# Performance work log

Measured on AMD Instinct MI355X. Metric: run time of the kernel, lower is better.

## Reference

```python
import jax, jax.numpy as jnp
import numpy as np

G = 512          # graphs in batch
NPG = 128        # nodes per graph (equal-sized so decoder batches)
TEMP = 0.1       # SimilarityDecoder temperature


def setup_inputs() -> dict:
    key = jax.random.key(0)
    ks = jax.random.split(key, 10)
    N, D, K, H, T = G * NPG, 512, 1024, 128, 10
    return {
        "x": jax.random.normal(ks[0], (N, D), jnp.float32),
        "batch": jnp.repeat(jnp.arange(G, dtype=jnp.int64), NPG),
        "codebook_input": jax.random.normal(ks[1], (K, D), jnp.float32),
        "fc1_w": jax.random.normal(ks[2], (H, D), jnp.float32) * (1.0 / np.sqrt(D)),
        "fc1_b": jax.random.normal(ks[3], (H,), jnp.float32) * 0.01,
        "fc2_w": jax.random.normal(ks[4], (D, H), jnp.float32) * (1.0 / np.sqrt(H)),
        "fc2_b": jax.random.normal(ks[5], (D,), jnp.float32) * 0.01,
        "causal": jax.random.normal(ks[6], (K, K), jnp.float32),
        "cls_w": jax.random.normal(ks[7], (T, D), jnp.float32) * (1.0 / np.sqrt(D)),
        "cls_b": jax.random.normal(ks[8], (T,), jnp.float32) * 0.01,
    }


def _segment_mean(v, batch, num_segments):
    s = jax.ops.segment_sum(v, batch, num_segments=num_segments)
    cnt = jax.ops.segment_sum(jnp.ones((v.shape[0], 1), v.dtype), batch, num_segments=num_segments)
    return s / jnp.maximum(cnt, 1.0)


def _batched_adj(z):
    # SimilarityDecoder: per-graph sigmoid(norm_z @ norm_z.T / temp); graphs equal-sized -> [G, n, n]
    zg = z.reshape(G, NPG, -1)
    zn = zg / jnp.maximum(jnp.linalg.norm(zg, axis=-1, keepdims=True), 1e-12)
    return jax.nn.sigmoid(jnp.einsum("gnd,gmd->gnm", zn, zn) / TEMP)


def reference(x, batch, codebook_input, fc1_w, fc1_b, fc2_w, fc2_b, causal, cls_w, cls_b):
    K = causal.shape[0]
    I = jnp.eye(K, dtype=x.dtype)

    # ---- VectorQuantizer ----
    h = jax.nn.sigmoid(codebook_input @ fc1_w.T + fc1_b)
    codebook_transformed = h @ fc2_w.T + fc2_b                 # [K, D]
    causal_effect = causal * (1.0 - I) + I                     # off-diag causal + identity
    cs = jax.nn.sigmoid(codebook_transformed)
    causal_diag = causal * I
    causal_cb = causal_effect @ (causal_diag @ cs)             # [K, D]
    counter_matrix = causal * (1.0 - I)                        # DegreeLayer assumed: off-diagonal mask
    counter_cb = causal_effect @ (counter_matrix @ cs)         # [K, D]

    # ---- ClassLayer ----
    pooled_x = _segment_mean(x, batch, G)                      # [G, D]
    # squared euclidean distances x vs causal_cb -> argmin codebook index
    d2 = (jnp.sum(x * x, 1, keepdims=True)
          - 2.0 * (x @ causal_cb.T)
          + jnp.sum(causal_cb * causal_cb, 1))                 # [N, K]
    idx = jnp.argmin(d2, axis=1)                               # [N]
    causal_nodes = x + causal_cb[idx]
    counter_nodes = counter_cb[idx]
    z_nodes = codebook_transformed[idx]                        # [N, D]
    pooled_causal = _segment_mean(causal_nodes, batch, G)
    pooled_counter = _segment_mean(counter_nodes, batch, G)
    causal_pre = pooled_causal @ cls_w.T + cls_b
    counter_pre = pooled_counter @ cls_w.T + cls_b
    y_pre = pooled_x @ jax.lax.stop_gradient(cls_w).T + jax.lax.stop_gradient(cls_b)

    # ---- SimilarityDecoder ----
    A_ori = _batched_adj(x)                                    # [G, n, n]
    A_rec = _batched_adj(z_nodes)

    return (causal_pre, counter_pre, y_pre, A_ori, A_rec,
            z_nodes, x, causal_diag, counter_matrix, pooled_causal, pooled_x)
```

## Files before the change

### kernel.cpp

```cpp
#include <hip/hip_runtime.h>
#include <math.h>

#define NG   512
#define NPG  128
#define NN   65536
#define DD   512
#define KK   1024
#define HH   128
#define TT   10

#define RES_TAU 1.0f
#define RES_CAP 65536

typedef __attribute__((ext_vector_type(8))) short short8;
typedef __attribute__((ext_vector_type(4))) float float4v;

static const long OFF_CPRE = 0;
static const long OFF_KPRE = 5120;
static const long OFF_YPRE = 10240;
static const long OFF_AORI = 15360;
static const long OFF_AREC = OFF_AORI + 8388608L;
static const long OFF_Z    = OFF_AREC + 8388608L;
static const long OFF_X    = OFF_Z + 33554432L;
static const long OFF_CD   = OFF_X + 33554432L;
static const long OFF_CM   = OFF_CD + 1048576L;
static const long OFF_PC   = OFF_CM + 1048576L;
static const long OFF_PX   = OFF_PC + 262144L;

__device__ __forceinline__ float sigm_fast(float v) { return 1.0f / (1.0f + __expf(-v)); }
__device__ __forceinline__ float sigm_acc (float v) { return 1.0f / (1.0f + expf(-v)); }

__global__ void k_diagmask(const float* __restrict__ causal,
                           float* __restrict__ cd, float* __restrict__ cm,
                           float* __restrict__ dv) {
  int i = blockIdx.x * 256 + threadIdx.x;
  int r = i >> 10, c = i & 1023;
  float v = causal[i];
  bool diag = (r == c);
  cd[i] = diag ? v : 0.0f;
  cm[i] = diag ? 0.0f : v;
  if (diag) dv[r] = v;
}

__global__ void k_fc1(const float* __restrict__ cbi, const float* __restrict__ w,
                      const float* __restrict__ b, float* __restrict__ h) {
  int i = blockIdx.x * 256 + threadIdx.x;
  int k = i >> 7, j = i & 127;
  const float4* xr = (const float4*)(cbi + (long)k * DD);
  const float4* wr = (const float4*)(w + (long)j * DD);
  float s = b[j];
  for (int d = 0; d < DD / 4; d++) {
    float4 a = xr[d], bb = wr[d];
    s += a.x * bb.x + a.y * bb.y + a.z * bb.z + a.w * bb.w;
  }
  h[i] = sigm_acc(s);
}

__global__ void k_fc2(const float* __restrict__ h, const float* __restrict__ w,
                      const float* __restrict__ b, float* __restrict__ ct,
                      float* __restrict__ cs) {
  int i = blockIdx.x * 256 + threadIdx.x;
  int k = i >> 9, d = i & 511;
  const float4* hr = (const float4*)(h + (long)k * HH);
  const float4* wr = (const float4*)(w + (long)d * HH);
  float s = b[d];
  for (int j = 0; j < HH / 4; j++) {
    float4 a = hr[j], bb = wr[j];
    s += a.x * bb.x + a.y * bb.y + a.z * bb.z + a.w * bb.w;
  }
  ct[i] = s;
  cs[i] = sigm_acc(s);
}

template <int AM, int BM>
__launch_bounds__(256)
__global__ void gemm64(const float* __restrict__ A, const float* __restrict__ B,
                       const float* __restrict__ dscale, float* __restrict__ C,
                       int M, int Nc, int Kr) {
  __shared__ __align__(16) float as[32][68];
  __shared__ __align__(16) float bs[32][68];
  int tid = threadIdx.x;
  int tx = tid & 15, ty = tid >> 4;
  int m0 = blockIdx.y * 64, n0 = blockIdx.x * 64;
  float acc[4][4] = {};
  for (int kt = 0; kt < Kr; kt += 32) {
    for (int s = tid; s < 512; s += 256) {
      int m = s >> 3, c4 = (s & 7) << 2;
      int gr = m0 + m, gc = kt + c4;
      float4 v = *(const float4*)&A[(long)gr * Kr + gc];
      float vv[4] = {v.x, v.y, v.z, v.w};
      if (AM == 1) {
#pragma unroll
        for (int q = 0; q < 4; q++) if (gc + q == gr) vv[q] = 1.0f;
      } else if (AM == 2) {
#pragma unroll
        for (int q = 0; q < 4; q++) if (gc + q == gr) vv[q] = 0.0f;
      }
      as[c4 + 0][m] = vv[0]; as[c4 + 1][m] = vv[1];
      as[c4 + 2][m] = vv[2]; as[c4 + 3][m] = vv[3];
    }
    for (int s = tid; s < 512; s += 256) {
      int r = s >> 4, c4 = (s & 15) << 2;
      float4 v = *(const float4*)&B[(long)(kt + r) * Nc + n0 + c4];
      if (BM == 1) {
        float sc = dscale[kt + r];
        v.x *= sc; v.y *= sc; v.z *= sc; v.w *= sc;
      }
      *(float4*)&bs[r][c4] = v;
    }
    __syncthreads();
#pragma unroll
    for (int r = 0; r < 32; r++) {
      float4 a4 = *(const float4*)&as[r][ty * 4];
      float4 b4 = *(const float4*)&bs[r][tx * 4];
      float av[4] = {a4.x, a4.y, a4.z, a4.w};
      float bv[4] = {b4.x, b4.y, b4.z, b4.w};
#pragma unroll
      for (int i = 0; i < 4; i++)
#pragma unroll
        for (int j = 0; j < 4; j++) acc[i][j] += av[i] * bv[j];
    }
    __syncthreads();
  }
#pragma unroll
  for (int i = 0; i < 4; i++) {
    float4 v = make_float4(acc[i][0], acc[i][1], acc[i][2], acc[i][3]);
    *(float4*)&C[(long)(m0 + ty * 4 + i) * Nc + n0 + tx * 4] = v;
  }
}

__global__ void k_cnorm(const float* __restrict__ ccb, float* __restrict__ cn2,
                        int* __restrict__ rc) {
  if (blockIdx.x == 0 && threadIdx.x == 0) *rc = 0;
  int row = blockIdx.x * 4 + (threadIdx.x >> 6);
  int lane = threadIdx.x & 63;
  const float* r = ccb + (long)row * DD;
  float s = 0.0f;
  for (int q = 0; q < DD; q += 64) { float v = r[lane + q]; s += v * v; }
  for (int off = 32; off > 0; off >>= 1) s += __shfl_down(s, off);
  if (lane == 0) cn2[row] = s;
}

__device__ __forceinline__ ushort bf16_rne(float f, float* back) {
  unsigned int b = __float_as_uint(f);
  unsigned int r = b + 0x7fffu + ((b >> 16) & 1u);
  ushort h = (ushort)(r >> 16);
  *back = __uint_as_float(((unsigned int)h) << 16);
  return h;
}

__global__ void k_split(const float4* __restrict__ src, ushort* __restrict__ hi,
                        ushort* __restrict__ lo, long n4) {
  long i = (long)blockIdx.x * 256 + threadIdx.x;
  if (i >= n4) return;
  float4 v = src[i];
  float vv[4] = {v.x, v.y, v.z, v.w};
  ushort h[4], l[4];
#pragma unroll
  for (int q = 0; q < 4; q++) {
    float back;
    h[q] = bf16_rne(vv[q], &back);
    float rem = vv[q] - back;
    float dummy;
    l[q] = bf16_rne(rem, &dummy);
  }
  ((ushort4*)hi)[i] = make_ushort4(h[0], h[1], h[2], h[3]);
  ((ushort4*)lo)[i] = make_ushort4(l[0], l[1], l[2], l[3]);
}

__launch_bounds__(512, 2)
__global__ void k_argmin_mfma(const ushort* __restrict__ xh, const ushort* __restrict__ xl,
                              const ushort* __restrict__ ch, const ushort* __restrict__ cl,
                              const float* __restrict__ cn2, int* __restrict__ idxg,
                              int* __restrict__ rc, int* __restrict__ rlist) {
  __shared__ __align__(16) ushort xsh[64 * 512];
  __shared__ __align__(16) ushort xsl[64 * 512];
  __shared__ float cn2s[KK];
  __shared__ float mm1[8][64], mm2[8][64];
  __shared__ int   mid[8][64];

  int tid = threadIdx.x;
  long n0 = (long)blockIdx.x * 64;

  uint4 tmp[16];
#pragma unroll
  for (int r = 0; r < 16; r++) {
    int g = tid + r * 512;
    int rid = g >> 6;
    int node = rid & 63;
    int gb = (g & 63) << 4;
    const ushort* src = ((rid < 64) ? xh : xl) + (n0 + node) * (long)DD;
    tmp[r] = *(const uint4*)((const char*)src + gb);
  }
  for (int s = tid; s < KK; s += 512) cn2s[s] = cn2[s];
#pragma unroll
  for (int r = 0; r < 16; r++) {
    int g = tid + r * 512;
    int rid = g >> 6;
    int node = rid & 63;
    int gb = (g & 63) << 4;
    int db = gb ^ ((node & 7) << 4);
    ushort* dst = (rid < 64) ? xsh : xsl;
    *(uint4*)((char*)dst + node * 1024 + db) = tmp[r];
  }
  __syncthreads();

  int lane = tid & 63, wave = tid >> 6;
  int col = lane & 15, quad = lane >> 4;

  int abase[4];
#pragma unroll
  for (int i = 0; i < 4; i++) {
    int node = i * 16 + col;
    abase[i] = node * 1024 + ((quad ^ (node & 3)) << 4) + (((node >> 2) & 1) << 6);
  }

  const ushort* pBh[4];
  const ushort* pBl[4];
#pragma unroll
  for (int j = 0; j < 4; j++) {
    long row = (long)(wave * 64 + j * 16 + col);
    pBh[j] = ch + row * DD + quad * 8;
    pBl[j] = cl + row * DD + quad * 8;
  }

  float m1[16], m2[16]; int id1[16];
#pragma unroll
  for (int s = 0; s < 16; s++) { m1[s] = 3.4e38f; m2[s] = 3.4e38f; id1[s] = 0; }

  const float4v vzero = {0.0f, 0.0f, 0.0f, 0.0f};
  float4v acc[4][4];
  short8 ahA[4], alA[4], bhA[4], blA[4];
  short8 ahB[4], alB[4], bhB[4], blB[4];

#define PREF(K, AH, AL, BH, BL)                                                  \
  do {                                                                           \
    int k_ = (K);                                                                \
    _Pragma("unroll") for (int j = 0; j < 4; j++) {                              \
      BH[j] = *(const short8*)(pBh[j] + k_ * 32);                                \
      BL[j] = *(const short8*)(pBl[j] + k_ * 32);                                \
    }                                                                            \
    _Pragma("unroll") for (int i = 0; i < 4; i++) {                              \
      int ao_ = abase[i] ^ (k_ << 6);                                            \
      AH[i] = *(const short8*)((const char*)xsh + ao_);                          \
      AL[i] = *(const short8*)((const char*)xsl + ao_);                          \
    }                                                                            \
  } while (0)

#define COMP(AH, AL, BH, BL)                                                     \
  do {                                                                           \
    __builtin_amdgcn_s_setprio(1);                                               \
    _Pragma("unroll") for (int j = 0; j < 4; j++)                                \
      _Pragma("unroll") for (int i = 0; i < 4; i++) {                            \
        acc[i][j] = __builtin_amdgcn_mfma_f32_16x16x32_bf16(AH[i], BH[j], acc[i][j], 0, 0, 0); \
        acc[i][j] = __builtin_amdgcn_mfma_f32_16x16x32_bf16(AH[i], BL[j], acc[i][j], 0, 0, 0); \
        acc[i][j] = __builtin_amdgcn_mfma_f32_16x16x32_bf16(AL[i], BH[j], acc[i][j], 0, 0, 0); \
      }                                                                          \
    __builtin_amdgcn_s_setprio(0);                                               \
  } while (0)

  for (int cc = 0; cc < 2; cc++) {
#pragma unroll
    for (int i = 0; i < 4; i++)
#pragma unroll
      for (int j = 0; j < 4; j++) acc[i][j] = vzero;

    PREF(0, ahA, alA, bhA, blA);
#pragma unroll 1
    for (int k = 0; k < 16; k += 2) {
      PREF(k + 1, ahB, alB, bhB, blB);
      COMP(ahA, alA, bhA, blA);
      PREF((k + 2) & 15, ahA, alA, bhA, blA);
      COMP(ahB, alB, bhB, blB);
    }

    int cb0 = cc * 512 + wave * 64;
#pragma unroll
    for (int j = 0; j < 4; j++) {
      int code = cb0 + j * 16 + col;
      float c2 = cn2s[code];
#pragma unroll
      for (int i = 0; i < 4; i++) {
#pragma unroll
        for (int r = 0; r < 4; r++) {
          float v = fmaf(-2.0f, acc[i][j][r], c2);
          int s = i * 4 + r;
          if (v < m1[s] || (v == m1[s] && code < id1[s])) {
            m2[s] = m1[s]; m1[s] = v; id1[s] = code;
          } else if (v < m2[s]) {
            m2[s] = v;
          }
        }
      }
    }
#pragma unroll
    for (int j = 0; j < 4; j++) { pBh[j] += 512 * DD; pBl[j] += 512 * DD; }
  }
#undef PREF
#undef COMP

#pragma unroll
  for (int s = 0; s < 16; s++) {
#pragma unroll
    for (int mask = 1; mask <= 8; mask <<= 1) {
      float om1 = __shfl_xor(m1[s], mask);
      float om2 = __shfl_xor(m2[s], mask);
      int   oid = __shfl_xor(id1[s], mask);
      if (om1 < m1[s] || (om1 == m1[s] && oid < id1[s])) {
        m2[s] = fminf(m1[s], om2); m1[s] = om1; id1[s] = oid;
      } else {
        m2[s] = fminf(m2[s], om1);
      }
    }
  }
  if (col == 0) {
#pragma unroll
    for (int s = 0; s < 16; s++) {
      int i = s >> 2, r = s & 3;
      int nl = i * 16 + quad * 4 + r;
      mm1[wave][nl] = m1[s]; mm2[wave][nl] = m2[s]; mid[wave][nl] = id1[s];
    }
  }
  __syncthreads();
  if (tid < 64) {
    float f1 = mm1[0][tid], f2 = mm2[0][tid]; int fi = mid[0][tid];
#pragma unroll
    for (int w = 1; w < 8; w++) {
      float b1 = mm1[w][tid], b2 = mm2[w][tid]; int bi = mid[w][tid];
      if (b1 < f1 || (b1 == f1 && bi < fi)) {
        f2 = fminf(f1, b2); f1 = b1; fi = bi;
      } else {
        f2 = fminf(f2, b1);
      }
    }
    idxg[n0 + tid] = fi;
    if (f2 - f1 < RES_TAU) {
      int p = atomicAdd(rc, 1);
      if (p < RES_CAP) rlist[p] = (int)(n0 + tid);
    }
  }
}

__global__ void k_rescue(const float* __restrict__ x, const float* __restrict__ ccb,
                         const float* __restrict__ cn2, const int* __restrict__ rc,
                         const int* __restrict__ rlist, int* __restrict__ idxg) {
  __shared__ float xs[DD];
  __shared__ float bv[256]; __shared__ int bi[256];
  int count = *rc; if (count > RES_CAP) count = RES_CAP;
  int tid = threadIdx.x;
  for (int f = blockIdx.x; f < count; f += gridDim.x) {
    int n = rlist[f];
    for (int s = tid; s < DD; s += 256) xs[s] = x[(long)n * DD + s];
    __syncthreads();
    float best = 3.4e38f; int besti = 0;
    for (int c = tid; c < KK; c += 256) {
      const float4* cr = (const float4*)(ccb + (long)c * DD);
      const float4* xr = (const float4*)xs;
      float dot = 0.0f;
      for (int d = 0; d < DD / 4; d++) {
        float4 a = xr[d], b = cr[d];
        dot += a.x * b.x + a.y * b.y + a.z * b.z + a.w * b.w;
      }
      float v = cn2[c] - 2.0f * dot;
      if (v < best || (v == best && c < besti)) { best = v; besti = c; }
    }
    bv[tid] = best; bi[tid] = besti;
    __syncthreads();
    for (int off = 128; off > 0; off >>= 1) {
      if (tid < off) {
        float ov = bv[tid + off]; int oi = bi[tid + off];
        if (ov < bv[tid] || (ov == bv[tid] && oi < bi[tid])) { bv[tid] = ov; bi[tid] = oi; }
      }
      __syncthreads();
    }
    if (tid == 0) idxg[n] = bi[0];
    __syncthreads();
  }
}

__global__ void k_gather(const float4* __restrict__ ct4, const int* __restrict__ idxg,
                         float4* __restrict__ z4) {
  long i = (long)blockIdx.x * 256 + threadIdx.x;
  int n = (int)(i >> 7), c = (int)(i & 127);
  z4[i] = ct4[(long)idxg[n] * 128 + c];
}

__global__ void k_pool(const float* __restrict__ x, const float* __restrict__ ccb,
                       const float* __restrict__ kcb, const int* __restrict__ idxg,
                       float* __restrict__ px, float* __restrict__ pc,
                       float* __restrict__ pk) {
  __shared__ int sidx[NPG];
  int g = blockIdx.x, tid = threadIdx.x;
  if (tid < NPG) sidx[tid] = idxg[g * NPG + tid];
  __syncthreads();
  int d = tid;
  float sx = 0.0f, sc = 0.0f, sk = 0.0f;
  for (int n = 0; n < NPG; n++) {
    sx += x[((long)g * NPG + n) * DD + d];
    long r = (long)sidx[n] * DD + d;
    sc += ccb[r]; sk += kcb[r];
  }
  px[(long)g * DD + d] = sx / 128.0f;
  pc[(long)g * DD + d] = (sx + sc) / 128.0f;
  pk[(long)g * DD + d] = sk / 128.0f;
}

__global__ void k_heads(const float* __restrict__ pc, const float* __restrict__ pk,
                        const float* __restrict__ px, const float* __restrict__ w,
                        const float* __restrict__ b, float* __restrict__ cpre,
                        float* __restrict__ kpre, float* __restrict__ ypre) {
  int g = blockIdx.x, t = threadIdx.x;
  if (t >= 30) return;
  int which = t / 10, tt = t % 10;
  const float* src = (which == 0) ? pc : ((which == 1) ? pk : px);
  const float* sr = src + (long)g * DD;
  const float* wr = w + (long)tt * DD;
  float s = 0.0f;
  for (int d = 0; d < DD; d++) s += sr[d] * wr[d];
  s += b[tt];
  float* dst = (which == 0) ? cpre : ((which == 1) ? kpre : ypre);
  dst[g * TT + tt] = s;
}

__global__ void k_copy(const float4* __restrict__ src, float4* __restrict__ dst) {
  long i = (long)blockIdx.x * 256 + threadIdx.x;
  dst[i] = src[i];
}

__launch_bounds__(256)
__global__ void k_adj(const float* __restrict__ Z, float* __restrict__ Aout) {
  __shared__ float nrm[NPG];
  __shared__ float inv[NPG];
  __shared__ __align__(16) float zs[32][132];
  int tid = threadIdx.x;
  int g = blockIdx.x;
  const float* base = Z + (long)g * NPG * DD;
  if (tid < NPG) nrm[tid] = 0.0f;
  __syncthreads();
  for (int k = 0; k < 64; k++) {
    long i = (long)k * 256 + tid;
    int n = (int)(i >> 7);
    float4 v = ((const float4*)base)[i];
    float s = v.x * v.x + v.y * v.y + v.z * v.z + v.w * v.w;
    for (int off = 32; off > 0; off >>= 1) s += __shfl_down(s, off);
    if ((tid & 63) == 0) atomicAdd(&nrm[n], s);
  }
  __syncthreads();
  if (tid < NPG) inv[tid] = 1.0f / fmaxf(sqrtf(nrm[tid]), 1e-12f);
  __syncthreads();
  float acc[8][8] = {};
  int tx = tid & 15, ty = tid >> 4;
  for (int dt = 0; dt < DD; dt += 32) {
    for (int s = tid; s < 1024; s += 256) {
      int n = s >> 3, c4 = (s & 7) << 2;
      float4 v = *(const float4*)&base[(long)n * DD + dt + c4];
      float iv = inv[n];
      zs[c4 + 0][n] = v.x * iv; zs[c4 + 1][n] = v.y * iv;
      zs[c4 + 2][n] = v.z * iv; zs[c4 + 3][n] = v.w * iv;
    }
    __syncthreads();
#pragma unroll 8
    for (int r = 0; r < 32; r++) {
      float rv[8], cv[8];
      *(float4*)&rv[0] = *(const float4*)&zs[r][ty * 8];
      *(float4*)&rv[4] = *(const float4*)&zs[r][ty * 8 + 4];
      *(float4*)&cv[0] = *(const float4*)&zs[r][tx * 8];
      *(float4*)&cv[4] = *(const float4*)&zs[r][tx * 8 + 4];
#pragma unroll
      for (int i = 0; i < 8; i++)
#pragma unroll
        for (int j = 0; j < 8; j++) acc[i][j] += rv[i] * cv[j];
    }
    __syncthreads();
  }
  float* aout = Aout + (long)g * NPG * NPG;
#pragma unroll
  for (int i = 0; i < 8; i++) {
    int rr = ty * 8 + i;
    float o[8];
#pragma unroll
    for (int j = 0; j < 8; j++) o[j] = sigm_fast(acc[i][j] * 10.0f);
    *(float4*)&aout[(long)rr * NPG + tx * 8]     = make_float4(o[0], o[1], o[2], o[3]);
    *(float4*)&aout[(long)rr * NPG + tx * 8 + 4] = make_float4(o[4], o[5], o[6], o[7]);
  }
}

extern "C" void kernel_launch(void* const* d_in, const int* in_sizes, int n_in,
                              void* d_out, int out_size, void* d_ws, size_t ws_size,
                              hipStream_t stream) {
  const float* x      = (const float*)d_in[0];
  const float* cbi    = (const float*)d_in[2];
  const float* fc1w   = (const float*)d_in[3];
  const float* fc1b   = (const float*)d_in[4];
  const float* fc2w   = (const float*)d_in[5];
  const float* fc2b   = (const float*)d_in[6];
  const float* causal = (const float*)d_in[7];
  const float* clsw   = (const float*)d_in[8];
  const float* clsb   = (const float*)d_in[9];
  float* out = (float*)d_out;

  float* cpre = out + OFF_CPRE;
  float* kpre = out + OFF_KPRE;
  float* ypre = out + OFF_YPRE;

  float* scr  = out + OFF_AORI;
  float* h    = scr;
  float* cs   = scr + 131072L;
  float* tmp2 = scr + 655360L;
  float* ccb  = scr + 1179648L;
  float* kcb  = scr + 1703936L;
  float* cn2  = scr + 2228224L;
  int*   idxg = (int*)(scr + 2229248L);
  float* pk   = scr + 2294784L;
  float* dv   = scr + 2556928L;
  ushort* ch  = (ushort*)(scr + 2557952L);
  ushort* cl  = (ushort*)(scr + 2820096L);
  int*   rc   = (int*)(scr + 3082240L);
  int*   rlist= (int*)(scr + 3082496L);
  float* ct   = out + OFF_AREC;
  ushort* xh  = (ushort*)(out + OFF_X);
  ushort* xl  = (ushort*)(out + OFF_X + 16777216L);

  k_diagmask<<<4096, 256, 0, stream>>>(causal, out + OFF_CD, out + OFF_CM, dv);
  k_fc1<<<512, 256, 0, stream>>>(cbi, fc1w, fc1b, h);
  k_fc2<<<2048, 256, 0, stream>>>(h, fc2w, fc2b, ct, cs);
  gemm64<2, 0><<<dim3(8, 16), 256, 0, stream>>>(causal, cs,   nullptr, tmp2, KK, DD, KK);
  gemm64<1, 1><<<dim3(8, 16), 256, 0, stream>>>(causal, cs,   dv,      ccb,  KK, DD, KK);
  gemm64<1, 0><<<dim3(8, 16), 256, 0, stream>>>(causal, tmp2, nullptr, kcb,  KK, DD, KK);
  k_cnorm<<<256, 256, 0, stream>>>(ccb, cn2, rc);
  k_split<<<32768, 256, 0, stream>>>((const float4*)x, xh, xl, 8388608L);
  k_split<<<512, 256, 0, stream>>>((const float4*)ccb, ch, cl, 131072L);
  k_argmin_mfma<<<1024, 512, 0, stream>>>(xh, xl, ch, cl, cn2, idxg, rc, rlist);
  k_rescue<<<128, 256, 0, stream>>>(x, ccb, cn2, rc, rlist, idxg);
  k_gather<<<32768, 256, 0, stream>>>((const float4*)ct, idxg, (float4*)(out + OFF_Z));
  k_pool<<<512, 512, 0, stream>>>(x, ccb, kcb, idxg, out + OFF_PX, out + OFF_PC, pk);
  k_heads<<<512, 64, 0, stream>>>(out + OFF_PC, pk, out + OFF_PX, clsw, clsb, cpre, kpre, ypre);
  k_copy<<<32768, 256, 0, stream>>>((const float4*)x, (float4*)(out + OFF_X));
  k_adj<<<512, 256, 0, stream>>>(out + OFF_Z, out + OFF_AREC);
  k_adj<<<512, 256, 0, stream>>>(x, out + OFF_AORI);
}
```

Baseline: 1.745 ms.

## Fuse two causal GEMMs, add nontemporal copies, restructure argmin MFMA pipeline

Two GEMMs that share the same causal matrix and cs operand are merged into one dual-accumulator kernel. Inside it, the A tile is masked once for the off-diagonal product and once for the identity diagonal, with a per-k scale applied to B. The x split and copy kernels and the argmin x loads now use nontemporal loads and stores to reduce cache pollution. The argmin inner loop is reorganised to load the A fragments from LDS just before use and to double-buffer only the B fragments, with sched_barriers fixing the order of loads and MFMAs. This lowers register pressure but gives the scheduler less freedom to interleave work.

```diff
diff --git a/kernel.cpp b/kernel.cpp
--- a/kernel.cpp
+++ b/kernel.cpp
@@ -14,6 +14,9 @@
 
 typedef __attribute__((ext_vector_type(8))) short short8;
 typedef __attribute__((ext_vector_type(4))) float float4v;
+typedef __attribute__((ext_vector_type(4))) float        f32x4;
+typedef __attribute__((ext_vector_type(4))) unsigned int u32x4;
+typedef __attribute__((ext_vector_type(4))) unsigned short u16x4;
 
 static const long OFF_CPRE = 0;
 static const long OFF_KPRE = 5120;
@@ -129,6 +132,70 @@
   }
 }
 
+__launch_bounds__(256)
+__global__ void gemm64_dual(const float* __restrict__ A, const float* __restrict__ B,
+                            const float* __restrict__ dscale,
+                            float* __restrict__ Cz, float* __restrict__ Ci,
+                            int M, int Nc, int Kr) {
+  __shared__ __align__(16) float asZ[32][68];
+  __shared__ __align__(16) float asI[32][68];
+  __shared__ __align__(16) float bs[32][68];
+  __shared__ float dsc[32];
+  int tid = threadIdx.x;
+  int tx = tid & 15, ty = tid >> 4;
+  int m0 = blockIdx.y * 64, n0 = blockIdx.x * 64;
+  float accZ[4][4] = {};
+  float accI[4][4] = {};
+  for (int kt = 0; kt < Kr; kt += 32) {
+    for (int s = tid; s < 512; s += 256) {
+      int m = s >> 3, c4 = (s & 7) << 2;
+      int gr = m0 + m, gc = kt + c4;
+      float4 v = *(const float4*)&A[(long)gr * Kr + gc];
+      float vz[4] = {v.x, v.y, v.z, v.w};
+      float vi[4] = {v.x, v.y, v.z, v.w};
+#pragma unroll
+      for (int q = 0; q < 4; q++) if (gc + q == gr) { vz[q] = 0.0f; vi[q] = 1.0f; }
+      asZ[c4 + 0][m] = vz[0]; asZ[c4 + 1][m] = vz[1];
+      asZ[c4 + 2][m] = vz[2]; asZ[c4 + 3][m] = vz[3];
+      asI[c4 + 0][m] = vi[0]; asI[c4 + 1][m] = vi[1];
+      asI[c4 + 2][m] = vi[2]; asI[c4 + 3][m] = vi[3];
+    }
+    for (int s = tid; s < 512; s += 256) {
+      int r = s >> 4, c4 = (s & 15) << 2;
+      float4 v = *(const float4*)&B[(long)(kt + r) * Nc + n0 + c4];
+      *(float4*)&bs[r][c4] = v;
+    }
+    if (tid < 32) dsc[tid] = dscale[kt + tid];
+    __syncthreads();
+#pragma unroll
+    for (int r = 0; r < 32; r++) {
+      float4 aZ = *(const float4*)&asZ[r][ty * 4];
+      float4 aI = *(const float4*)&asI[r][ty * 4];
+      float4 b4 = *(const float4*)&bs[r][tx * 4];
+      float sc = dsc[r];
+      float az[4] = {aZ.x, aZ.y, aZ.z, aZ.w};
+      float ai[4] = {aI.x, aI.y, aI.z, aI.w};
+      float bz[4] = {b4.x, b4.y, b4.z, b4.w};
+      float bi[4] = {b4.x * sc, b4.y * sc, b4.z * sc, b4.w * sc};
+#pragma unroll
+      for (int i = 0; i < 4; i++)
+#pragma unroll
+        for (int j = 0; j < 4; j++) {
+          accZ[i][j] += az[i] * bz[j];
+          accI[i][j] += ai[i] * bi[j];
+        }
+    }
+    __syncthreads();
+  }
+#pragma unroll
+  for (int i = 0; i < 4; i++) {
+    float4 vz = make_float4(accZ[i][0], accZ[i][1], accZ[i][2], accZ[i][3]);
+    float4 vi = make_float4(accI[i][0], accI[i][1], accI[i][2], accI[i][3]);
+    *(float4*)&Cz[(long)(m0 + ty * 4 + i) * Nc + n0 + tx * 4] = vz;
+    *(float4*)&Ci[(long)(m0 + ty * 4 + i) * Nc + n0 + tx * 4] = vi;
+  }
+}
+
 __global__ void k_cnorm(const float* __restrict__ ccb, float* __restrict__ cn2,
                         int* __restrict__ rc) {
   if (blockIdx.x == 0 && threadIdx.x == 0) *rc = 0;
@@ -168,6 +235,26 @@
   ((ushort4*)lo)[i] = make_ushort4(l[0], l[1], l[2], l[3]);
 }
 
+__global__ void k_split_nt(const float* __restrict__ src, ushort* __restrict__ hi,
+                           ushort* __restrict__ lo, long n4) {
+  long i = (long)blockIdx.x * 256 + threadIdx.x;
+  if (i >= n4) return;
+  f32x4 v = __builtin_nontemporal_load((const f32x4*)src + i);
+  ushort h[4], l[4];
+#pragma unroll
+  for (int q = 0; q < 4; q++) {
+    float back;
+    h[q] = bf16_rne(v[q], &back);
+    float rem = v[q] - back;
+    float dummy;
+    l[q] = bf16_rne(rem, &dummy);
+  }
+  u16x4 hv = {h[0], h[1], h[2], h[3]};
+  u16x4 lv = {l[0], l[1], l[2], l[3]};
+  __builtin_nontemporal_store(hv, (u16x4*)hi + i);
+  __builtin_nontemporal_store(lv, (u16x4*)lo + i);
+}
+
 __launch_bounds__(512, 2)
 __global__ void k_argmin_mfma(const ushort* __restrict__ xh, const ushort* __restrict__ xl,
                               const ushort* __restrict__ ch, const ushort* __restrict__ cl,
@@ -182,7 +269,7 @@
   int tid = threadIdx.x;
   long n0 = (long)blockIdx.x * 64;
 
-  uint4 tmp[16];
+  u32x4 tmp[16];
 #pragma unroll
   for (int r = 0; r < 16; r++) {
     int g = tid + r * 512;
@@ -190,7 +277,7 @@
     int node = rid & 63;
     int gb = (g & 63) << 4;
     const ushort* src = ((rid < 64) ? xh : xl) + (n0 + node) * (long)DD;
-    tmp[r] = *(const uint4*)((const char*)src + gb);
+    tmp[r] = __builtin_nontemporal_load((const u32x4*)((const char*)src + gb));
   }
   for (int s = tid; s < KK; s += 512) cn2s[s] = cn2[s];
 #pragma unroll
@@ -201,7 +288,7 @@
     int gb = (g & 63) << 4;
     int db = gb ^ ((node & 7) << 4);
     ushort* dst = (rid < 64) ? xsh : xsl;
-    *(uint4*)((char*)dst + node * 1024 + db) = tmp[r];
+    *(u32x4*)((char*)dst + node * 1024 + db) = tmp[r];
   }
   __syncthreads();
 
@@ -230,31 +317,36 @@
 
   const float4v vzero = {0.0f, 0.0f, 0.0f, 0.0f};
   float4v acc[4][4];
-  short8 ahA[4], alA[4], bhA[4], blA[4];
-  short8 ahB[4], alB[4], bhB[4], blB[4];
-
-#define PREF(K, AH, AL, BH, BL)                                                  \
+  short8 aH[4], aL[4];
+  short8 bh0[4], bl0[4], bh1[4], bl1[4];
+
+#define LDA(K)                                                                   \
+  do {                                                                           \
+    int k_ = (K);                                                                \
+    _Pragma("unroll") for (int i = 0; i < 4; i++) {                              \
+      int ao_ = abase[i] ^ (k_ << 6);                                            \
+      aH[i] = *(const short8*)((const char*)xsh + ao_);                          \
+      aL[i] = *(const short8*)((const char*)xsl + ao_);                          \
+    }                                                                            \
+  } while (0)
+
+#define LDB(K, BH, BL)                                                           \
   do {                                                                           \
     int k_ = (K);                                                                \
     _Pragma("unroll") for (int j = 0; j < 4; j++) {                              \
       BH[j] = *(const short8*)(pBh[j] + k_ * 32);                                \
       BL[j] = *(const short8*)(pBl[j] + k_ * 32);                                \
     }                                                                            \
-    _Pragma("unroll") for (int i = 0; i < 4; i++) {                              \
-      int ao_ = abase[i] ^ (k_ << 6);                                            \
-      AH[i] = *(const short8*)((const char*)xsh + ao_);                          \
-      AL[i] = *(const short8*)((const char*)xsl + ao_);                          \
-    }                                                                            \
   } while (0)
 
-#define COMP(AH, AL, BH, BL)                                                     \
+#define COMP(BH, BL)                                                             \
   do {                                                                           \
     __builtin_amdgcn_s_setprio(1);                                               \
     _Pragma("unroll") for (int j = 0; j < 4; j++)                                \
       _Pragma("unroll") for (int i = 0; i < 4; i++) {                            \
-        acc[i][j] = __builtin_amdgcn_mfma_f32_16x16x32_bf16(AH[i], BH[j], acc[i][j], 0, 0, 0); \
-        acc[i][j] = __builtin_amdgcn_mfma_f32_16x16x32_bf16(AH[i], BL[j], acc[i][j], 0, 0, 0); \
-        acc[i][j] = __builtin_amdgcn_mfma_f32_16x16x32_bf16(AL[i], BH[j], acc[i][j], 0, 0, 0); \
+        acc[i][j] = __builtin_amdgcn_mfma_f32_16x16x32_bf16(aH[i], BH[j], acc[i][j], 0, 0, 0); \
+        acc[i][j] = __builtin_amdgcn_mfma_f32_16x16x32_bf16(aH[i], BL[j], acc[i][j], 0, 0, 0); \
+        acc[i][j] = __builtin_amdgcn_mfma_f32_16x16x32_bf16(aL[i], BH[j], acc[i][j], 0, 0, 0); \
       }                                                                          \
     __builtin_amdgcn_s_setprio(0);                                               \
   } while (0)
@@ -265,13 +357,19 @@
 #pragma unroll
       for (int j = 0; j < 4; j++) acc[i][j] = vzero;
 
-    PREF(0, ahA, alA, bhA, blA);
+    LDB(0, bh0, bl0);
 #pragma unroll 1
     for (int k = 0; k < 16; k += 2) {
-      PREF(k + 1, ahB, alB, bhB, blB);
-      COMP(ahA, alA, bhA, blA);
-      PREF((k + 2) & 15, ahA, alA, bhA, blA);
-      COMP(ahB, alB, bhB, blB);
+      LDA(k);
+      LDB(k + 1, bh1, bl1);
+      __builtin_amdgcn_sched_barrier(0);
+      COMP(bh0, bl0);
+      __builtin_amdgcn_sched_barrier(0);
+      LDA(k + 1);
+      LDB((k + 2) & 15, bh0, bl0);
+      __builtin_amdgcn_sched_barrier(0);
+      COMP(bh1, bl1);
+      __builtin_amdgcn_sched_barrier(0);
     }
 
     int cb0 = cc * 512 + wave * 64;
@@ -296,7 +394,8 @@
 #pragma unroll
     for (int j = 0; j < 4; j++) { pBh[j] += 512 * DD; pBl[j] += 512 * DD; }
   }
-#undef PREF
+#undef LDA
+#undef LDB
 #undef COMP
 
 #pragma unroll
@@ -422,9 +521,10 @@
   dst[g * TT + tt] = s;
 }
 
-__global__ void k_copy(const float4* __restrict__ src, float4* __restrict__ dst) {
+__global__ void k_copy(const float* __restrict__ src, float* __restrict__ dst) {
   long i = (long)blockIdx.x * 256 + threadIdx.x;
-  dst[i] = src[i];
+  f32x4 v = __builtin_nontemporal_load((const f32x4*)src + i);
+  __builtin_nontemporal_store(v, (f32x4*)dst + i);
 }
 
 __launch_bounds__(256)
@@ -524,18 +624,17 @@
   k_diagmask<<<4096, 256, 0, stream>>>(causal, out + OFF_CD, out + OFF_CM, dv);
   k_fc1<<<512, 256, 0, stream>>>(cbi, fc1w, fc1b, h);
   k_fc2<<<2048, 256, 0, stream>>>(h, fc2w, fc2b, ct, cs);
-  gemm64<2, 0><<<dim3(8, 16), 256, 0, stream>>>(causal, cs,   nullptr, tmp2, KK, DD, KK);
-  gemm64<1, 1><<<dim3(8, 16), 256, 0, stream>>>(causal, cs,   dv,      ccb,  KK, DD, KK);
-  gemm64<1, 0><<<dim3(8, 16), 256, 0, stream>>>(causal, tmp2, nullptr, kcb,  KK, DD, KK);
+  gemm64_dual<<<dim3(8, 16), 256, 0, stream>>>(causal, cs, dv, tmp2, ccb, KK, DD, KK);
+  gemm64<1, 0><<<dim3(8, 16), 256, 0, stream>>>(causal, tmp2, nullptr, kcb, KK, DD, KK);
   k_cnorm<<<256, 256, 0, stream>>>(ccb, cn2, rc);
-  k_split<<<32768, 256, 0, stream>>>((const float4*)x, xh, xl, 8388608L);
+  k_split_nt<<<32768, 256, 0, stream>>>(x, xh, xl, 8388608L);
   k_split<<<512, 256, 0, stream>>>((const float4*)ccb, ch, cl, 131072L);
   k_argmin_mfma<<<1024, 512, 0, stream>>>(xh, xl, ch, cl, cn2, idxg, rc, rlist);
   k_rescue<<<128, 256, 0, stream>>>(x, ccb, cn2, rc, rlist, idxg);
   k_gather<<<32768, 256, 0, stream>>>((const float4*)ct, idxg, (float4*)(out + OFF_Z));
   k_pool<<<512, 512, 0, stream>>>(x, ccb, kcb, idxg, out + OFF_PX, out + OFF_PC, pk);
   k_heads<<<512, 64, 0, stream>>>(out + OFF_PC, pk, out + OFF_PX, clsw, clsb, cpre, kpre, ypre);
-  k_copy<<<32768, 256, 0, stream>>>((const float4*)x, (float4*)(out + OFF_X));
+  k_copy<<<32768, 256, 0, stream>>>(x, out + OFF_X);
   k_adj<<<512, 256, 0, stream>>>(out + OFF_Z, out + OFF_AREC);
   k_adj<<<512, 256, 0, stream>>>(x, out + OFF_AORI);
 }
```

Measured after the change: 1.680 ms. 1.04x faster.
